# Optimization experiments

Hardware: AMD Instinct MI355X
Metric: run time of the kernel (lower is better)

## Reference

```python
import jax, jax.numpy as jnp
import numpy as np

B, H, NI, NO, T = 128, 256, 2, 10, 64
LAMBDA, ETA, SAMPLE, DECISION = 0.95, 0.5, 32, 8


def _xavier(key, shape):
    fan_in, fan_out = shape
    s = (2.0 / (fan_in + fan_out)) ** 0.5
    return jax.random.normal(key, shape, dtype=jnp.float32) * s


def setup_inputs():
    key = jax.random.key(0)
    ks = jax.random.split(key, 10)
    return {
        "x_in": jax.random.normal(ks[0], (T, B, 5), dtype=jnp.float32),
        "W_sr": _xavier(ks[1], (NI, H)),
        "W_ma": _xavier(ks[2], (NI + 1, H)),
        "W_ro": _xavier(ks[3], (H, H)),
        "W_ao": _xavier(ks[4], (H, H)),
        "W_ar": _xavier(ks[5], (H, H)),
        "W_ra": _xavier(ks[6], (H, H)),
        "W_a": _xavier(ks[7], (H, H)),
        "W_y": _xavier(ks[8], (H, NO)),
        "g": jnp.ones((1, H), dtype=jnp.float32),
        "b": jnp.zeros((1, H), dtype=jnp.float32),
        "time": T,
    }


def _forward(x_in, W_sr, W_ma, W_ro, W_ao, W_ar, W_ra, W_a, W_y, g, b):
    Tn = x_in.shape[0]

    def step(carry, inp):
        r, a, A = carry
        x, t = inp  # x: [B,5]
        a_prev = a
        # ATN / RSC recurrent populations
        a = jax.nn.relu(x[:, NI:] @ W_ma + a @ W_a + r @ W_ra)      # [B,H]
        r = jax.nn.relu(x[:, :NI] @ W_sr + a_prev @ W_ar)           # [B,H]
        # readout through fast-weight memory A: o = ro(r) + r @ A + ao(a)
        o = r @ W_ro + jnp.einsum('bh,bhk->bk', r, A) + a @ W_ao    # [B,H]
        mu = jnp.mean(o, axis=0, keepdims=True)                     # mean over batch
        o = jax.nn.relu(g * (o - mu) + b)
        # Hebbian fast-weight update: A = lambda*A + eta * outer(o, r)
        eta_t = jnp.where(t > SAMPLE, 0.0, ETA)
        A = LAMBDA * A + eta_t * o[:, :, None] * r[:, None, :]      # [B,H,H]
        y = o @ W_y                                                 # [B,NO]
        return (r, a, A), y

    carry0 = (
        jnp.zeros((B, H), jnp.float32),
        jnp.zeros((B, H), jnp.float32),
        jnp.zeros((B, H, H), jnp.float32),
    )
    _, ys = jax.lax.scan(step, carry0, (x_in, jnp.arange(Tn)))
    return ys[-DECISION:]  # [decision, B, n_output]


def reference(x_in, W_sr, W_ma, W_ro, W_ao, W_ar, W_ra, W_a, W_y, g, b, time):
    return _forward(x_in, W_sr, W_ma, W_ro, W_ao, W_ar, W_ra, W_a, W_y, g, b)
```

## Files before the change

kernel.cpp:

```cpp
#include <hip/hip_runtime.h>


typedef unsigned long long u64;

#define HH 256
#define NSTEPS 64

#define OFF_ST 0u
#define OFF_C  262144u
#define OFF_MU 329728u
#define WS_FLOATS 395264u

#define SENT_STATE   0xBF800000BF800000ull
#define SENT_C       0xBF800000u
#define SENT_MU      0x7FC00000u
#define SENT_MU_PAIR 0x7FC000007FC00000ull

#define AGENT __HIP_MEMORY_SCOPE_AGENT
#define RLX   __ATOMIC_RELAXED

__device__ __forceinline__ u64 ld64(const u64* p){ return __hip_atomic_load(p,RLX,AGENT); }
__device__ __forceinline__ void st64s(u64* p,u64 v){ __hip_atomic_store(p,v,RLX,AGENT); }
__device__ __forceinline__ float ld32f(const float* p){ return __hip_atomic_load(p,RLX,AGENT); }
__device__ __forceinline__ void st32f(float* p,float v){ __hip_atomic_store(p,v,RLX,AGENT); }
__device__ __forceinline__ u64 pack2(float lo,float hi){
  return (u64)__float_as_uint(lo) | ((u64)__float_as_uint(hi)<<32);
}

__global__ __launch_bounds__(256) void smn_init(float* __restrict__ ws,
                                                float* __restrict__ out){
  unsigned i = blockIdx.x*256u + threadIdx.x, st = gridDim.x*256u;
  u64* stp=(u64*)(ws+OFF_ST); float* cp=ws+OFF_C; u64* mp=(u64*)(ws+OFF_MU);
  for (unsigned k=i;k<131072u;k+=st) st64s(&stp[k],SENT_STATE);
  for (unsigned k=i;k<67584u;k+=st)  st32f(&cp[k],-1.0f);
  for (unsigned k=i;k<32768u;k+=st)  st64s(&mp[k],SENT_MU_PAIR);
  for (unsigned k=i;k<10240u;k+=st)  out[k]=0.f;
}

__global__ __launch_bounds__(512) void smn_main(
    const float* __restrict__ x_in, const float* __restrict__ W_sr,
    const float* __restrict__ W_ma, const float* __restrict__ W_ro,
    const float* __restrict__ W_ao, const float* __restrict__ W_ar,
    const float* __restrict__ W_ra, const float* __restrict__ W_a,
    const float* __restrict__ W_y,  const float* __restrict__ gvec,
    const float* __restrict__ bvec, float* __restrict__ out,
    float* __restrict__ ws)
{
  __shared__ __align__(16) float aF[2][HH], rF[2][HH];
  __shared__ __align__(16) float P[2][32][2][64];
  __shared__ __align__(16) float r_hist[33][2][64];
  __shared__ __align__(16) float o_hist[33][2][64];
  __shared__ float a_own[2][64], r_own[2][64];
  __shared__ float opre[2][64];
  __shared__ float c_l[33][2];
  __shared__ float mu_l[64];
  __shared__ float muG[16][32][2];
  __shared__ float lam_pow[64];
  __shared__ float x_l[2][5];
  __shared__ float lds_pad[8192];

  const int tid = threadIdx.x;
  const int bid = blockIdx.x;
  const int grp = bid >> 2, jsl = bid & 3;
  const int b0 = grp * 2, c0 = jsl * 64;
  const int q = tid & 15, ks = tid >> 4;

  u64*   st64    = (u64*)(ws + OFF_ST);
  float* c_parts = ws + OFF_C;
  u64*   mu64    = (u64*)(ws + OFF_MU);

  if (out == nullptr) lds_pad[tid] = 1.f;

  const int cc = c0 + (tid & 63);
  const float gv  = gvec[cc], bv = bvec[cc];
  const float wma0=W_ma[cc], wma1=W_ma[HH+cc], wma2=W_ma[2*HH+cc];
  const float wsr0=W_sr[cc], wsr1=W_sr[HH+cc];
  if (tid < 64) lam_pow[tid] = powf(0.95f,(float)tid);
  if (tid < 10) x_l[tid/5][tid%5] = x_in[(b0 + tid/5)*5 + tid%5];
  __syncthreads();

  for (int t = 0; t <= NSTEPS; ++t) {
    if (t < NSTEPS) {
      if (t == 0) {
        if (tid < 128) {
          int b = tid>>6, c = tid&63;
          float va = fmaxf(x_l[b][2]*wma0 + x_l[b][3]*wma1 + x_l[b][4]*wma2, 0.f);
          float vr = fmaxf(x_l[b][0]*wsr0 + x_l[b][1]*wsr1, 0.f);
          a_own[b][c]=va; r_own[b][c]=vr; r_hist[0][b][c]=vr;
          st64s(&st64[(unsigned)((b0+b)*HH + cc)], pack2(va,vr));
        }
        __syncthreads();
      } else {
        const int kb = ks*8;
        float sa0[8],sa1[8],sr0[8],sr1[8];
        *(float4*)&sa0[0]=*(const float4*)&aF[0][kb]; *(float4*)&sa0[4]=*(const float4*)&aF[0][kb+4];
        *(float4*)&sa1[0]=*(const float4*)&aF[1][kb]; *(float4*)&sa1[4]=*(const float4*)&aF[1][kb+4];
        *(float4*)&sr0[0]=*(const float4*)&rF[0][kb]; *(float4*)&sr0[4]=*(const float4*)&rF[0][kb+4];
        *(float4*)&sr1[0]=*(const float4*)&rF[1][kb]; *(float4*)&sr1[4]=*(const float4*)&rF[1][kb+4];
        float aA[2][4]={{0.f,0.f,0.f,0.f},{0.f,0.f,0.f,0.f}};
        float aR[2][4]={{0.f,0.f,0.f,0.f},{0.f,0.f,0.f,0.f}};
        #pragma unroll
        for (int kk=0; kk<8; ++kk) {
          const int k = kb + kk;
          const float4 wa = *(const float4*)&W_a [k*HH + c0 + q*4];
          const float4 wr = *(const float4*)&W_ra[k*HH + c0 + q*4];
          const float4 wn = *(const float4*)&W_ar[k*HH + c0 + q*4];
          #pragma unroll
          for (int jj=0;jj<4;++jj){
            const float waj=(&wa.x)[jj], wrj=(&wr.x)[jj], wnj=(&wn.x)[jj];
            aA[0][jj] += sa0[kk]*waj + sr0[kk]*wrj;
            aA[1][jj] += sa1[kk]*waj + sr1[kk]*wrj;
            aR[0][jj] += sa0[kk]*wnj;
            aR[1][jj] += sa1[kk]*wnj;
          }
        }
        *(float4*)&P[0][ks][0][q*4] = make_float4(aA[0][0],aA[0][1],aA[0][2],aA[0][3]);
        *(float4*)&P[0][ks][1][q*4] = make_float4(aA[1][0],aA[1][1],aA[1][2],aA[1][3]);
        *(float4*)&P[1][ks][0][q*4] = make_float4(aR[0][0],aR[0][1],aR[0][2],aR[0][3]);
        *(float4*)&P[1][ks][1][q*4] = make_float4(aR[1][0],aR[1][1],aR[1][2],aR[1][3]);
        __syncthreads();
        if (tid < 128) {
          int b=tid>>6, c=tid&63;
          float sa=0.f, sr=0.f;
          #pragma unroll
          for (int e=0;e<32;++e){ sa+=P[0][e][b][c]; sr+=P[1][e][b][c]; }
          float va = fmaxf(sa + x_l[b][2]*wma0 + x_l[b][3]*wma1 + x_l[b][4]*wma2, 0.f);
          float vr = fmaxf(sr + x_l[b][0]*wsr0 + x_l[b][1]*wsr1, 0.f);
          a_own[b][c]=va; r_own[b][c]=vr;
          if (t<=32) r_hist[t][b][c]=vr;
          st64s(&st64[(unsigned)((t&3)*32768) + (unsigned)((b0+b)*HH + cc)], pack2(va,vr));
        }
        __syncthreads();
      }
      if (t+1 < NSTEPS && tid < 10)
        x_l[tid/5][tid%5] = x_in[((t+1)*128 + b0 + tid/5)*5 + tid%5];
    }

    const int tp = t - 1;
    const bool fin = (t >= 1) && (tp <= 32 || tp >= 56);
    if (fin) {
      const int m = (tp <= 32) ? tp : tp - 23;
      {
        const int p = tid & 31, ch = tid >> 5;
        const u64* base = &mu64[(unsigned)(((m&3)*4 + jsl)*64) * 32u];
        float s0=0.f, s1=0.f;
        #pragma unroll
        for (int gg=0; gg<4; ++gg) {
          const u64* ptr = &base[(unsigned)((ch*4+gg)*32 + p)];
          u64 v;
          for (;;){ v = ld64(ptr);
            if ((unsigned)v != SENT_MU && (unsigned)(v>>32) != SENT_MU) break;
            __builtin_amdgcn_s_sleep(1);
          }
          s0 += __uint_as_float((unsigned)v);
          s1 += __uint_as_float((unsigned)(v>>32));
        }
        muG[ch][p][0]=s0; muG[ch][p][1]=s1;
      }
      __syncthreads();
      if (tid < 32) {
        float s0=0.f,s1=0.f;
        #pragma unroll
        for (int ch2=0;ch2<16;++ch2){ s0+=muG[ch2][tid][0]; s1+=muG[ch2][tid][1]; }
        mu_l[2*tid]=s0*(1.f/128.f); mu_l[2*tid+1]=s1*(1.f/128.f);
        st64s(&mu64[(unsigned)((((m+3)&3)*4 + jsl)*64 + grp)*32u + (unsigned)tid], SENT_MU_PAIR);
      }
      __syncthreads();
      if (tid < 128) {
        int b=tid>>6, c=tid&63;
        float o = fmaxf(gv*(opre[b][c]-mu_l[c]) + bv, 0.f);
        opre[b][c]=o;
        if (tp<=32) o_hist[tp][b][c]=o;
      }
      __syncthreads();
      if (tp >= 56 && tid < 320) {
        int ow=tid>>4, l16=tid&15, b=ow/10, n=ow%10;
        float acc=0.f;
        #pragma unroll
        for (int i2=0;i2<4;++i2){ int c=l16*4+i2; acc += opre[b][c]*W_y[(c0+c)*10+n]; }
        acc+=__shfl_xor(acc,1); acc+=__shfl_xor(acc,2);
        acc+=__shfl_xor(acc,4); acc+=__shfl_xor(acc,8);
        if (l16==0) atomicAdd(&out[(tp-56)*1280 + (b0+b)*10 + n], acc);
      }
    }
    if (t == NSTEPS) break;

    const bool live = (t <= 32 || t >= 56);
    const int mc = (t <= 32) ? t : t - 23;
    const int smax = (t-1 < 32) ? (t-1) : 32;

    if (tid < 128) {
      if (live && smax >= 0) {
        const int l8 = tid & 7;
        for (int pp = tid>>3; pp < (smax+1)*2; pp += 16) {
          const int s = pp>>1, b = pp&1;
          float acc=0.f;
          #pragma unroll
          for (int i2=0;i2<8;++i2){ int c=l8*8+i2; acc += r_own[b][c]*o_hist[s][b][c]; }
          acc+=__shfl_xor(acc,1); acc+=__shfl_xor(acc,2); acc+=__shfl_xor(acc,4);
          if (l8==0) st32f(&c_parts[(unsigned)((((mc&3)*33+s)*128 + b0+b)*4 + jsl)], acc);
        }
      }
      { int b=tid>>6, c=tid&63; aF[b][c0+c]=a_own[b][c]; rF[b][c0+c]=r_own[b][c]; }
    } else {
      const int w = tid - 128;
      const int pi = w >> 7, w2 = w & 127, b = w2>>6, c64 = w2&63;
      const int jp = (jsl + 1 + pi) & 3;
      const u64* ptr = &st64[(unsigned)((t&3)*32768) + (unsigned)((b0+b)*HH + jp*64 + c64)];
      u64 v;
      for (;;){ v = ld64(ptr); if (v != SENT_STATE) break; }
      aF[b][jp*64+c64] = __uint_as_float((unsigned)v);
      rF[b][jp*64+c64] = __uint_as_float((unsigned)(v>>32));
    }
    __syncthreads();
    if (tid < 128) {
      int b=tid>>6;
      st64s(&st64[(unsigned)(((t+3)&3)*32768) + (unsigned)((b0+b)*HH + cc)], SENT_STATE);
    }

    if (live) {
      const int kb = ks*8;
      float sa0[8],sa1[8],sr0[8],sr1[8];
      *(float4*)&sa0[0]=*(const float4*)&aF[0][kb]; *(float4*)&sa0[4]=*(const float4*)&aF[0][kb+4];
      *(float4*)&sa1[0]=*(const float4*)&aF[1][kb]; *(float4*)&sa1[4]=*(const float4*)&aF[1][kb+4];
      *(float4*)&sr0[0]=*(const float4*)&rF[0][kb]; *(float4*)&sr0[4]=*(const float4*)&rF[0][kb+4];
      *(float4*)&sr1[0]=*(const float4*)&rF[1][kb]; *(float4*)&sr1[4]=*(const float4*)&rF[1][kb+4];
      float aO[2][4]={{0.f,0.f,0.f,0.f},{0.f,0.f,0.f,0.f}};
      #pragma unroll
      for (int kk=0;kk<8;++kk){
        const int k=kb+kk;
        const float4 wo=*(const float4*)&W_ro[k*HH + c0 + q*4];
        const float4 wq=*(const float4*)&W_ao[k*HH + c0 + q*4];
        #pragma unroll
        for (int jj=0;jj<4;++jj){
          aO[0][jj] += sr0[kk]*(&wo.x)[jj] + sa0[kk]*(&wq.x)[jj];
          aO[1][jj] += sr1[kk]*(&wo.x)[jj] + sa1[kk]*(&wq.x)[jj];
        }
      }
      *(float4*)&P[0][ks][0][q*4] = make_float4(aO[0][0],aO[0][1],aO[0][2],aO[0][3]);
      *(float4*)&P[0][ks][1][q*4] = make_float4(aO[1][0],aO[1][1],aO[1][2],aO[1][3]);
      if (smax >= 0 && tid < (smax+1)*8) {
        const int s=tid>>3, b=(tid>>2)&1, jj2=tid&3;
        const float* ptr=&c_parts[(unsigned)((((mc&3)*33+s)*128 + b0+b)*4 + jj2)];
        float v;
        for(;;){ v=ld32f(ptr); if (__float_as_uint(v)!=SENT_C) break; }
        v+=__shfl_xor(v,1); v+=__shfl_xor(v,2);
        if (jj2==0) c_l[s][b]=v;
      }
      __syncthreads();
      if (smax >= 0 && tid >= 128 && tid < 194) {
        const int s=(tid-128)>>1, b=(tid-128)&1;
        st32f(&c_parts[(unsigned)(((((mc+3)&3)*33+s)*128 + b0+b)*4 + jsl)], -1.0f);
      }
      if (tid < 128) {
        int b=tid>>6, c=tid&63;
        float s=0.f;
        #pragma unroll
        for (int e=0;e<32;++e) s+=P[0][e][b][c];
        for (int s2=0;s2<=smax;++s2)
          s += lam_pow[t-1-s2]*0.5f*c_l[s2][b]*r_hist[s2][b][c];
        opre[b][c]=s;
      }
      __syncthreads();
      if (tid < 32) {
        float plo=opre[0][2*tid]+opre[1][2*tid];
        float phi=opre[0][2*tid+1]+opre[1][2*tid+1];
        st64s(&mu64[(unsigned)(((mc&3)*4 + jsl)*64 + grp)*32u + (unsigned)tid], pack2(plo,phi));
      }
    }
  }
}

extern "C" void kernel_launch(void* const* d_in, const int* in_sizes, int n_in,
                              void* d_out, int out_size, void* d_ws, size_t ws_size,
                              hipStream_t stream) {
  if (ws_size < (size_t)WS_FLOATS * 4) return;
  const float* x_in = (const float*)d_in[0];
  const float* W_sr = (const float*)d_in[1];
  const float* W_ma = (const float*)d_in[2];
  const float* W_ro = (const float*)d_in[3];
  const float* W_ao = (const float*)d_in[4];
  const float* W_ar = (const float*)d_in[5];
  const float* W_ra = (const float*)d_in[6];
  const float* W_a  = (const float*)d_in[7];
  const float* W_y  = (const float*)d_in[8];
  const float* g    = (const float*)d_in[9];
  const float* b    = (const float*)d_in[10];
  float* out = (float*)d_out;
  float* ws  = (float*)d_ws;

  hipLaunchKernelGGL(smn_init, dim3(256), dim3(256), 0, stream, ws, out);
  hipLaunchKernelGGL(smn_main, dim3(256), dim3(512), 0, stream,
                     x_in, W_sr, W_ma, W_ro, W_ao, W_ar, W_ra, W_a, W_y, g, b,
                     out, ws);
}
```

Measured before the change: 366.7 us.

## Split hidden dimension across 8 blocks per batch pair with smaller workgroups

Each batch pair's hidden columns are now split across 8 blocks of 256 threads, 32 columns each, instead of 4 blocks of 512 threads with 64 columns. The LDS padding array is removed so two workgroups can share a CU, and the launch grows to 512 blocks. Cross-block polling for state and mu now issues several independent loads per pass instead of one load with a sleep between retries. The intent is to cut per-block work on the serial recurrence critical path. The cost is more inter-block communication, since each block gathers 7 remote slices per step, and the reduction scratch buffers become twice as large.

```diff
diff --git a/kernel.cpp b/kernel.cpp
--- a/kernel.cpp
+++ b/kernel.cpp
@@ -8,8 +8,8 @@
 
 #define OFF_ST 0u
 #define OFF_C  262144u
-#define OFF_MU 329728u
-#define WS_FLOATS 395264u
+#define OFF_MU 397312u
+#define WS_FLOATS 462848u
 
 #define SENT_STATE   0xBF800000BF800000ull
 #define SENT_C       0xBF800000u
@@ -32,12 +32,12 @@
   unsigned i = blockIdx.x*256u + threadIdx.x, st = gridDim.x*256u;
   u64* stp=(u64*)(ws+OFF_ST); float* cp=ws+OFF_C; u64* mp=(u64*)(ws+OFF_MU);
   for (unsigned k=i;k<131072u;k+=st) st64s(&stp[k],SENT_STATE);
-  for (unsigned k=i;k<67584u;k+=st)  st32f(&cp[k],-1.0f);
+  for (unsigned k=i;k<135168u;k+=st) st32f(&cp[k],__uint_as_float(SENT_C));
   for (unsigned k=i;k<32768u;k+=st)  st64s(&mp[k],SENT_MU_PAIR);
   for (unsigned k=i;k<10240u;k+=st)  out[k]=0.f;
 }
 
-__global__ __launch_bounds__(512) void smn_main(
+__global__ __launch_bounds__(256,2) void smn_main(
     const float* __restrict__ x_in, const float* __restrict__ W_sr,
     const float* __restrict__ W_ma, const float* __restrict__ W_ro,
     const float* __restrict__ W_ao, const float* __restrict__ W_ar,
@@ -47,34 +47,30 @@
     float* __restrict__ ws)
 {
   __shared__ __align__(16) float aF[2][HH], rF[2][HH];
-  __shared__ __align__(16) float P[2][32][2][64];
-  __shared__ __align__(16) float r_hist[33][2][64];
-  __shared__ __align__(16) float o_hist[33][2][64];
-  __shared__ float a_own[2][64], r_own[2][64];
-  __shared__ float opre[2][64];
+  __shared__ __align__(16) float P[2][32][2][32];
+  __shared__ __align__(16) float r_hist[33][2][32];
+  __shared__ __align__(16) float o_hist[33][2][32];
+  __shared__ float opre[2][32];
   __shared__ float c_l[33][2];
-  __shared__ float mu_l[64];
-  __shared__ float muG[16][32][2];
+  __shared__ float mu_l[32];
+  __shared__ float muG[16][16][2];
   __shared__ float lam_pow[64];
   __shared__ float x_l[2][5];
-  __shared__ float lds_pad[8192];
 
   const int tid = threadIdx.x;
   const int bid = blockIdx.x;
-  const int grp = bid >> 2, jsl = bid & 3;
-  const int b0 = grp * 2, c0 = jsl * 64;
-  const int q = tid & 15, ks = tid >> 4;
+  const int grp = bid >> 3, jsl = bid & 7;
+  const int b0 = grp * 2, c0 = jsl * 32;
+  const int q = tid & 7, ks = tid >> 3;
 
   u64*   st64    = (u64*)(ws + OFF_ST);
   float* c_parts = ws + OFF_C;
   u64*   mu64    = (u64*)(ws + OFF_MU);
 
-  if (out == nullptr) lds_pad[tid] = 1.f;
-
-  const int cc = c0 + (tid & 63);
-  const float gv  = gvec[cc], bv = bvec[cc];
-  const float wma0=W_ma[cc], wma1=W_ma[HH+cc], wma2=W_ma[2*HH+cc];
-  const float wsr0=W_sr[cc], wsr1=W_sr[HH+cc];
+  const int cc2 = c0 + (tid & 31);
+  const float gv  = gvec[cc2], bv = bvec[cc2];
+  const float wma0=W_ma[cc2], wma1=W_ma[HH+cc2], wma2=W_ma[2*HH+cc2];
+  const float wsr0=W_sr[cc2], wsr1=W_sr[HH+cc2];
   if (tid < 64) lam_pow[tid] = powf(0.95f,(float)tid);
   if (tid < 10) x_l[tid/5][tid%5] = x_in[(b0 + tid/5)*5 + tid%5];
   __syncthreads();
@@ -82,12 +78,12 @@
   for (int t = 0; t <= NSTEPS; ++t) {
     if (t < NSTEPS) {
       if (t == 0) {
-        if (tid < 128) {
-          int b = tid>>6, c = tid&63;
+        if (tid < 64) {
+          int b = tid>>5, c = tid&31;
           float va = fmaxf(x_l[b][2]*wma0 + x_l[b][3]*wma1 + x_l[b][4]*wma2, 0.f);
           float vr = fmaxf(x_l[b][0]*wsr0 + x_l[b][1]*wsr1, 0.f);
-          a_own[b][c]=va; r_own[b][c]=vr; r_hist[0][b][c]=vr;
-          st64s(&st64[(unsigned)((b0+b)*HH + cc)], pack2(va,vr));
+          aF[b][c0+c]=va; rF[b][c0+c]=vr; r_hist[0][b][c]=vr;
+          st64s(&st64[(unsigned)((b0+b)*HH + cc2)], pack2(va,vr));
         }
         __syncthreads();
       } else {
@@ -119,16 +115,16 @@
         *(float4*)&P[1][ks][0][q*4] = make_float4(aR[0][0],aR[0][1],aR[0][2],aR[0][3]);
         *(float4*)&P[1][ks][1][q*4] = make_float4(aR[1][0],aR[1][1],aR[1][2],aR[1][3]);
         __syncthreads();
-        if (tid < 128) {
-          int b=tid>>6, c=tid&63;
+        if (tid < 64) {
+          int b=tid>>5, c=tid&31;
           float sa=0.f, sr=0.f;
           #pragma unroll
           for (int e=0;e<32;++e){ sa+=P[0][e][b][c]; sr+=P[1][e][b][c]; }
           float va = fmaxf(sa + x_l[b][2]*wma0 + x_l[b][3]*wma1 + x_l[b][4]*wma2, 0.f);
           float vr = fmaxf(sr + x_l[b][0]*wsr0 + x_l[b][1]*wsr1, 0.f);
-          a_own[b][c]=va; r_own[b][c]=vr;
           if (t<=32) r_hist[t][b][c]=vr;
-          st64s(&st64[(unsigned)((t&3)*32768) + (unsigned)((b0+b)*HH + cc)], pack2(va,vr));
+          st64s(&st64[(unsigned)((t&3)*32768) + (unsigned)((b0+b)*HH + cc2)], pack2(va,vr));
+          aF[b][c0+c]=va; rF[b][c0+c]=vr;
         }
         __syncthreads();
       }
@@ -141,46 +137,51 @@
     if (fin) {
       const int m = (tp <= 32) ? tp : tp - 23;
       {
-        const int p = tid & 31, ch = tid >> 5;
-        const u64* base = &mu64[(unsigned)(((m&3)*4 + jsl)*64) * 32u];
+        const int p = tid & 15, ch = tid >> 4;
+        const u64* base = &mu64[(unsigned)(((m&3)*8 + jsl)*64)*16u];
+        u64 vals[4]; unsigned rm = 0;
+        const u64* ptrs[4];
+        #pragma unroll
+        for (int gg=0; gg<4; ++gg) ptrs[gg] = &base[(unsigned)((ch*4+gg)*16 + p)];
+        while (rm != 0xFu) {
+          #pragma unroll
+          for (int gg=0; gg<4; ++gg) if (!(rm & (1u<<gg))) {
+            u64 v = ld64(ptrs[gg]);
+            if ((unsigned)v != SENT_MU && (unsigned)(v>>32) != SENT_MU) { vals[gg]=v; rm |= 1u<<gg; }
+          }
+        }
         float s0=0.f, s1=0.f;
         #pragma unroll
-        for (int gg=0; gg<4; ++gg) {
-          const u64* ptr = &base[(unsigned)((ch*4+gg)*32 + p)];
-          u64 v;
-          for (;;){ v = ld64(ptr);
-            if ((unsigned)v != SENT_MU && (unsigned)(v>>32) != SENT_MU) break;
-            __builtin_amdgcn_s_sleep(1);
-          }
-          s0 += __uint_as_float((unsigned)v);
-          s1 += __uint_as_float((unsigned)(v>>32));
-        }
+        for (int gg=0; gg<4; ++gg) { s0 += __uint_as_float((unsigned)vals[gg]);
+                                     s1 += __uint_as_float((unsigned)(vals[gg]>>32)); }
         muG[ch][p][0]=s0; muG[ch][p][1]=s1;
       }
       __syncthreads();
-      if (tid < 32) {
+      if (tid < 16) {
         float s0=0.f,s1=0.f;
         #pragma unroll
         for (int ch2=0;ch2<16;++ch2){ s0+=muG[ch2][tid][0]; s1+=muG[ch2][tid][1]; }
         mu_l[2*tid]=s0*(1.f/128.f); mu_l[2*tid+1]=s1*(1.f/128.f);
-        st64s(&mu64[(unsigned)((((m+3)&3)*4 + jsl)*64 + grp)*32u + (unsigned)tid], SENT_MU_PAIR);
-      }
-      __syncthreads();
-      if (tid < 128) {
-        int b=tid>>6, c=tid&63;
+        st64s(&mu64[(unsigned)((((m+3)&3)*8 + jsl)*64 + grp)*16u + (unsigned)tid], SENT_MU_PAIR);
+      }
+      __syncthreads();
+      if (tid < 64) {
+        int b=tid>>5, c=tid&31;
         float o = fmaxf(gv*(opre[b][c]-mu_l[c]) + bv, 0.f);
         opre[b][c]=o;
         if (tp<=32) o_hist[tp][b][c]=o;
       }
       __syncthreads();
-      if (tp >= 56 && tid < 320) {
-        int ow=tid>>4, l16=tid&15, b=ow/10, n=ow%10;
-        float acc=0.f;
-        #pragma unroll
-        for (int i2=0;i2<4;++i2){ int c=l16*4+i2; acc += opre[b][c]*W_y[(c0+c)*10+n]; }
-        acc+=__shfl_xor(acc,1); acc+=__shfl_xor(acc,2);
-        acc+=__shfl_xor(acc,4); acc+=__shfl_xor(acc,8);
-        if (l16==0) atomicAdd(&out[(tp-56)*1280 + (b0+b)*10 + n], acc);
+      if (tp >= 56) {
+        const int pr = tid>>3, l8 = tid&7;
+        if (pr < 20) {
+          const int b = pr/10, n = pr%10;
+          float acc=0.f;
+          #pragma unroll
+          for (int i2=0;i2<4;++i2){ int c=l8*4+i2; acc += opre[b][c]*W_y[(c0+c)*10+n]; }
+          acc+=__shfl_xor(acc,1); acc+=__shfl_xor(acc,2); acc+=__shfl_xor(acc,4);
+          if (l8==0) atomicAdd(&out[(tp-56)*1280 + (b0+b)*10 + n], acc);
+        }
       }
     }
     if (t == NSTEPS) break;
@@ -189,33 +190,52 @@
     const int mc = (t <= 32) ? t : t - 23;
     const int smax = (t-1 < 32) ? (t-1) : 32;
 
-    if (tid < 128) {
-      if (live && smax >= 0) {
-        const int l8 = tid & 7;
-        for (int pp = tid>>3; pp < (smax+1)*2; pp += 16) {
+    const int gbase = live ? 128 : 0;
+    if (live && tid < 128) {
+      if (smax >= 0) {
+        const int l4 = tid & 3;
+        for (int pp = tid>>2; pp < (smax+1)*2; pp += 32) {
           const int s = pp>>1, b = pp&1;
           float acc=0.f;
           #pragma unroll
-          for (int i2=0;i2<8;++i2){ int c=l8*8+i2; acc += r_own[b][c]*o_hist[s][b][c]; }
-          acc+=__shfl_xor(acc,1); acc+=__shfl_xor(acc,2); acc+=__shfl_xor(acc,4);
-          if (l8==0) st32f(&c_parts[(unsigned)((((mc&3)*33+s)*128 + b0+b)*4 + jsl)], acc);
-        }
-      }
-      { int b=tid>>6, c=tid&63; aF[b][c0+c]=a_own[b][c]; rF[b][c0+c]=r_own[b][c]; }
-    } else {
-      const int w = tid - 128;
-      const int pi = w >> 7, w2 = w & 127, b = w2>>6, c64 = w2&63;
-      const int jp = (jsl + 1 + pi) & 3;
-      const u64* ptr = &st64[(unsigned)((t&3)*32768) + (unsigned)((b0+b)*HH + jp*64 + c64)];
-      u64 v;
-      for (;;){ v = ld64(ptr); if (v != SENT_STATE) break; }
-      aF[b][jp*64+c64] = __uint_as_float((unsigned)v);
-      rF[b][jp*64+c64] = __uint_as_float((unsigned)(v>>32));
+          for (int i2=0;i2<8;++i2){ int c=l4*8+i2; acc += rF[b][c0+c]*o_hist[s][b][c]; }
+          acc+=__shfl_xor(acc,1); acc+=__shfl_xor(acc,2);
+          if (l4==0) st32f(&c_parts[(unsigned)((((mc&3)*33+s)*128 + b0+b)*8 + jsl)], acc);
+        }
+      }
+    }
+    if (tid >= gbase) {
+      const int gstep = live ? 128 : 256;
+      const int w0 = tid - gbase;
+      const u64* ptrs[4]; int bs[4], cs[4]; bool ok[4];
+      u64 vals[4]; unsigned rm = 0;
+      #pragma unroll
+      for (int i=0;i<4;++i) {
+        int w = w0 + i*gstep;
+        bool valid = (w < 512);
+        int b = (w>>8)&1, c = w&255;
+        ok[i] = valid && ((c>>5) != jsl);
+        bs[i]=b; cs[i]=c;
+        ptrs[i] = &st64[(unsigned)((t&3)*32768) + (unsigned)((b0+b)*HH + c)];
+        if (!ok[i]) rm |= 1u<<i;
+      }
+      while (rm != 0xFu) {
+        #pragma unroll
+        for (int i=0;i<4;++i) if (!(rm & (1u<<i))) {
+          u64 v = ld64(ptrs[i]);
+          if (v != SENT_STATE) { vals[i]=v; rm |= 1u<<i; }
+        }
+      }
+      #pragma unroll
+      for (int i=0;i<4;++i) if (ok[i]) {
+        aF[bs[i]][cs[i]] = __uint_as_float((unsigned)vals[i]);
+        rF[bs[i]][cs[i]] = __uint_as_float((unsigned)(vals[i]>>32));
+      }
     }
     __syncthreads();
-    if (tid < 128) {
-      int b=tid>>6;
-      st64s(&st64[(unsigned)(((t+3)&3)*32768) + (unsigned)((b0+b)*HH + cc)], SENT_STATE);
+    if (tid < 64) {
+      int b=tid>>5;
+      st64s(&st64[(unsigned)(((t+3)&3)*32768) + (unsigned)((b0+b)*HH + cc2)], SENT_STATE);
     }
 
     if (live) {
@@ -239,21 +259,25 @@
       }
       *(float4*)&P[0][ks][0][q*4] = make_float4(aO[0][0],aO[0][1],aO[0][2],aO[0][3]);
       *(float4*)&P[0][ks][1][q*4] = make_float4(aO[1][0],aO[1][1],aO[1][2],aO[1][3]);
-      if (smax >= 0 && tid < (smax+1)*8) {
-        const int s=tid>>3, b=(tid>>2)&1, jj2=tid&3;
-        const float* ptr=&c_parts[(unsigned)((((mc&3)*33+s)*128 + b0+b)*4 + jj2)];
-        float v;
-        for(;;){ v=ld32f(ptr); if (__float_as_uint(v)!=SENT_C) break; }
-        v+=__shfl_xor(v,1); v+=__shfl_xor(v,2);
-        if (jj2==0) c_l[s][b]=v;
-      }
-      __syncthreads();
-      if (smax >= 0 && tid >= 128 && tid < 194) {
-        const int s=(tid-128)>>1, b=(tid-128)&1;
-        st32f(&c_parts[(unsigned)(((((mc+3)&3)*33+s)*128 + b0+b)*4 + jsl)], -1.0f);
-      }
-      if (tid < 128) {
-        int b=tid>>6, c=tid&63;
+      if (smax >= 0) {
+        const int jj2 = tid & 7;
+        for (int pp = tid>>3; pp < (smax+1)*2; pp += 32) {
+          const int s=pp>>1, b=pp&1;
+          const float* ptr=&c_parts[(unsigned)((((mc&3)*33+s)*128 + b0+b)*8 + jj2)];
+          float v;
+          for(;;){ v=ld32f(ptr); if (__float_as_uint(v)!=SENT_C) break; }
+          v+=__shfl_xor(v,1); v+=__shfl_xor(v,2); v+=__shfl_xor(v,4);
+          if (jj2==0) c_l[s][b]=v;
+        }
+      }
+      __syncthreads();
+      if (smax >= 0 && tid >= 64 && tid < 64 + (smax+1)*2) {
+        const int s=(tid-64)>>1, b=(tid-64)&1;
+        st32f(&c_parts[(unsigned)(((((mc+3)&3)*33+s)*128 + b0+b)*8 + jsl)],
+              __uint_as_float(SENT_C));
+      }
+      if (tid < 64) {
+        int b=tid>>5, c=tid&31;
         float s=0.f;
         #pragma unroll
         for (int e=0;e<32;++e) s+=P[0][e][b][c];
@@ -262,10 +286,10 @@
         opre[b][c]=s;
       }
       __syncthreads();
-      if (tid < 32) {
+      if (tid < 16) {
         float plo=opre[0][2*tid]+opre[1][2*tid];
         float phi=opre[0][2*tid+1]+opre[1][2*tid+1];
-        st64s(&mu64[(unsigned)(((mc&3)*4 + jsl)*64 + grp)*32u + (unsigned)tid], pack2(plo,phi));
+        st64s(&mu64[(unsigned)(((mc&3)*8 + jsl)*64 + grp)*16u + (unsigned)tid], pack2(plo,phi));
       }
     }
   }
@@ -290,7 +314,7 @@
   float* ws  = (float*)d_ws;
 
   hipLaunchKernelGGL(smn_init, dim3(256), dim3(256), 0, stream, ws, out);
-  hipLaunchKernelGGL(smn_main, dim3(256), dim3(512), 0, stream,
+  hipLaunchKernelGGL(smn_main, dim3(512), dim3(256), 0, stream,
                      x_in, W_sr, W_ma, W_ro, W_ao, W_ar, W_ra, W_a, W_y, g, b,
                      out, ws);
 }
```

New measurement: 482.1 us. +31.5%, slower.

## Reschedule cross-block exchange, prefetch readout weights, and use lighter LDS barriers

Applied to the files above, without the earlier changes.

Reorders the per-step schedule so the state exchange and the Hebbian c-partial computation run before the mean reduction rather than after. The readout weights W_ro/W_ao are prefetched into registers ahead of the mu spin-wait, and sentinel resets are moved to the producer side two slots ahead. The four mu slots are polled concurrently without sleeping. Several __syncthreads calls become an s_waitcnt lgkmcnt(0) plus s_barrier, and launch bounds now request two blocks per SIMD. The goal is shorter critical-path latency per timestep in this spin-synchronised persistent kernel. The cost is more register pressure and fragile ordering of the sentinel protocol.

```diff
diff --git a/kernel.cpp b/kernel.cpp
--- a/kernel.cpp
+++ b/kernel.cpp
@@ -18,6 +18,8 @@
 
 #define AGENT __HIP_MEMORY_SCOPE_AGENT
 #define RLX   __ATOMIC_RELAXED
+
+#define BAR_LGKM() asm volatile("s_waitcnt lgkmcnt(0)\ns_barrier" ::: "memory")
 
 __device__ __forceinline__ u64 ld64(const u64* p){ return __hip_atomic_load(p,RLX,AGENT); }
 __device__ __forceinline__ void st64s(u64* p,u64 v){ __hip_atomic_store(p,v,RLX,AGENT); }
@@ -32,12 +34,12 @@
   unsigned i = blockIdx.x*256u + threadIdx.x, st = gridDim.x*256u;
   u64* stp=(u64*)(ws+OFF_ST); float* cp=ws+OFF_C; u64* mp=(u64*)(ws+OFF_MU);
   for (unsigned k=i;k<131072u;k+=st) st64s(&stp[k],SENT_STATE);
-  for (unsigned k=i;k<67584u;k+=st)  st32f(&cp[k],-1.0f);
+  for (unsigned k=i;k<67584u;k+=st)  st32f(&cp[k],__uint_as_float(SENT_C));
   for (unsigned k=i;k<32768u;k+=st)  st64s(&mp[k],SENT_MU_PAIR);
   for (unsigned k=i;k<10240u;k+=st)  out[k]=0.f;
 }
 
-__global__ __launch_bounds__(512) void smn_main(
+__global__ __launch_bounds__(512,2) void smn_main(
     const float* __restrict__ x_in, const float* __restrict__ W_sr,
     const float* __restrict__ W_ma, const float* __restrict__ W_ro,
     const float* __restrict__ W_ao, const float* __restrict__ W_ar,
@@ -50,7 +52,6 @@
   __shared__ __align__(16) float P[2][32][2][64];
   __shared__ __align__(16) float r_hist[33][2][64];
   __shared__ __align__(16) float o_hist[33][2][64];
-  __shared__ float a_own[2][64], r_own[2][64];
   __shared__ float opre[2][64];
   __shared__ float c_l[33][2];
   __shared__ float mu_l[64];
@@ -71,25 +72,29 @@
 
   if (out == nullptr) lds_pad[tid] = 1.f;
 
-  const int cc = c0 + (tid & 63);
-  const float gv  = gvec[cc], bv = bvec[cc];
-  const float wma0=W_ma[cc], wma1=W_ma[HH+cc], wma2=W_ma[2*HH+cc];
-  const float wsr0=W_sr[cc], wsr1=W_sr[HH+cc];
+  const int cc2 = c0 + (tid & 63);
+  const float gv  = gvec[cc2], bv = bvec[cc2];
+  const float wma0=W_ma[cc2], wma1=W_ma[HH+cc2], wma2=W_ma[2*HH+cc2];
+  const float wsr0=W_sr[cc2], wsr1=W_sr[HH+cc2];
   if (tid < 64) lam_pow[tid] = powf(0.95f,(float)tid);
   if (tid < 10) x_l[tid/5][tid%5] = x_in[(b0 + tid/5)*5 + tid%5];
   __syncthreads();
 
   for (int t = 0; t <= NSTEPS; ++t) {
+    const bool live = (t <= 32 || t >= 56);
+    const int mc = (t <= 32) ? t : t - 23;
+
     if (t < NSTEPS) {
       if (t == 0) {
         if (tid < 128) {
           int b = tid>>6, c = tid&63;
           float va = fmaxf(x_l[b][2]*wma0 + x_l[b][3]*wma1 + x_l[b][4]*wma2, 0.f);
           float vr = fmaxf(x_l[b][0]*wsr0 + x_l[b][1]*wsr1, 0.f);
-          a_own[b][c]=va; r_own[b][c]=vr; r_hist[0][b][c]=vr;
-          st64s(&st64[(unsigned)((b0+b)*HH + cc)], pack2(va,vr));
-        }
-        __syncthreads();
+          aF[b][c0+c]=va; rF[b][c0+c]=vr; r_hist[0][b][c]=vr;
+          st64s(&st64[(unsigned)(2*32768) + (unsigned)((b0+b)*HH + cc2)], SENT_STATE);
+          st64s(&st64[(unsigned)((b0+b)*HH + cc2)], pack2(va,vr));
+        }
+        BAR_LGKM();
       } else {
         const int kb = ks*8;
         float sa0[8],sa1[8],sr0[8],sr1[8];
@@ -118,7 +123,7 @@
         *(float4*)&P[0][ks][1][q*4] = make_float4(aA[1][0],aA[1][1],aA[1][2],aA[1][3]);
         *(float4*)&P[1][ks][0][q*4] = make_float4(aR[0][0],aR[0][1],aR[0][2],aR[0][3]);
         *(float4*)&P[1][ks][1][q*4] = make_float4(aR[1][0],aR[1][1],aR[1][2],aR[1][3]);
-        __syncthreads();
+        BAR_LGKM();
         if (tid < 128) {
           int b=tid>>6, c=tid&63;
           float sa=0.f, sr=0.f;
@@ -126,38 +131,82 @@
           for (int e=0;e<32;++e){ sa+=P[0][e][b][c]; sr+=P[1][e][b][c]; }
           float va = fmaxf(sa + x_l[b][2]*wma0 + x_l[b][3]*wma1 + x_l[b][4]*wma2, 0.f);
           float vr = fmaxf(sr + x_l[b][0]*wsr0 + x_l[b][1]*wsr1, 0.f);
-          a_own[b][c]=va; r_own[b][c]=vr;
           if (t<=32) r_hist[t][b][c]=vr;
-          st64s(&st64[(unsigned)((t&3)*32768) + (unsigned)((b0+b)*HH + cc)], pack2(va,vr));
-        }
-        __syncthreads();
+          st64s(&st64[(unsigned)(((t+2)&3)*32768) + (unsigned)((b0+b)*HH + cc2)], SENT_STATE);
+          st64s(&st64[(unsigned)((t&3)*32768) + (unsigned)((b0+b)*HH + cc2)], pack2(va,vr));
+          aF[b][c0+c]=va; rF[b][c0+c]=vr;
+        }
+        BAR_LGKM();
       }
       if (t+1 < NSTEPS && tid < 10)
         x_l[tid/5][tid%5] = x_in[((t+1)*128 + b0 + tid/5)*5 + tid%5];
     }
 
+    float4 woR[8], wqR[8];
+    if (t < NSTEPS && live) {
+      const int kb = ks*8;
+      #pragma unroll
+      for (int kk=0;kk<8;++kk){
+        woR[kk] = *(const float4*)&W_ro[(kb+kk)*HH + c0 + q*4];
+        wqR[kk] = *(const float4*)&W_ao[(kb+kk)*HH + c0 + q*4];
+      }
+    }
+
+    if (t < NSTEPS) {
+      const int smax_old = ((t-2) < 32) ? (t-2) : 32;
+      if (tid < 128) {
+        if (live && smax_old >= 0) {
+          const int l8 = tid & 7;
+          for (int pp = tid>>3; pp < (smax_old+1)*2; pp += 16) {
+            const int s = pp>>1, b2 = pp&1;
+            float acc=0.f;
+            #pragma unroll
+            for (int i2=0;i2<8;++i2){ int c=l8*8+i2; acc += rF[b2][c0+c]*o_hist[s][b2][c]; }
+            acc+=__shfl_xor(acc,1); acc+=__shfl_xor(acc,2); acc+=__shfl_xor(acc,4);
+            if (l8==0) {
+              st32f(&c_parts[(unsigned)(((((mc+2)&3)*33+s)*128 + b0+b2)*4 + jsl)],
+                    __uint_as_float(SENT_C));
+              st32f(&c_parts[(unsigned)((((mc&3)*33+s)*128 + b0+b2)*4 + jsl)], acc);
+            }
+          }
+        }
+      } else {
+        const int w = tid - 128;
+        const int pi = w >> 7, w2 = w & 127, b = w2>>6, c64 = w2&63;
+        const int jp = (jsl + 1 + pi) & 3;
+        const u64* ptr = &st64[(unsigned)((t&3)*32768) + (unsigned)((b0+b)*HH + jp*64 + c64)];
+        u64 v;
+        for (;;){ v = ld64(ptr); if (v != SENT_STATE) break; }
+        aF[b][jp*64+c64] = __uint_as_float((unsigned)v);
+        rF[b][jp*64+c64] = __uint_as_float((unsigned)(v>>32));
+      }
+      if (live) { BAR_LGKM(); } else { __syncthreads(); }
+    }
+
     const int tp = t - 1;
-    const bool fin = (t >= 1) && (tp <= 32 || tp >= 56);
-    if (fin) {
+    if (t >= 1 && (tp <= 32 || tp >= 56)) {
       const int m = (tp <= 32) ? tp : tp - 23;
       {
         const int p = tid & 31, ch = tid >> 5;
-        const u64* base = &mu64[(unsigned)(((m&3)*4 + jsl)*64) * 32u];
+        const u64* base = &mu64[(unsigned)(((m&3)*4 + jsl)*64)*32u];
+        u64 vals[4]; unsigned rm = 0;
+        const u64* ptrs[4];
+        #pragma unroll
+        for (int gg=0; gg<4; ++gg) ptrs[gg] = &base[(unsigned)((ch*4+gg)*32 + p)];
+        while (rm != 0xFu) {
+          #pragma unroll
+          for (int gg=0; gg<4; ++gg) if (!(rm & (1u<<gg))) {
+            u64 v = ld64(ptrs[gg]);
+            if ((unsigned)v != SENT_MU && (unsigned)(v>>32) != SENT_MU) { vals[gg]=v; rm |= 1u<<gg; }
+          }
+        }
         float s0=0.f, s1=0.f;
         #pragma unroll
-        for (int gg=0; gg<4; ++gg) {
-          const u64* ptr = &base[(unsigned)((ch*4+gg)*32 + p)];
-          u64 v;
-          for (;;){ v = ld64(ptr);
-            if ((unsigned)v != SENT_MU && (unsigned)(v>>32) != SENT_MU) break;
-            __builtin_amdgcn_s_sleep(1);
-          }
-          s0 += __uint_as_float((unsigned)v);
-          s1 += __uint_as_float((unsigned)(v>>32));
-        }
+        for (int gg=0; gg<4; ++gg) { s0 += __uint_as_float((unsigned)vals[gg]);
+                                     s1 += __uint_as_float((unsigned)(vals[gg]>>32)); }
         muG[ch][p][0]=s0; muG[ch][p][1]=s1;
       }
-      __syncthreads();
+      BAR_LGKM();
       if (tid < 32) {
         float s0=0.f,s1=0.f;
         #pragma unroll
@@ -165,14 +214,14 @@
         mu_l[2*tid]=s0*(1.f/128.f); mu_l[2*tid+1]=s1*(1.f/128.f);
         st64s(&mu64[(unsigned)((((m+3)&3)*4 + jsl)*64 + grp)*32u + (unsigned)tid], SENT_MU_PAIR);
       }
-      __syncthreads();
+      BAR_LGKM();
       if (tid < 128) {
         int b=tid>>6, c=tid&63;
         float o = fmaxf(gv*(opre[b][c]-mu_l[c]) + bv, 0.f);
         opre[b][c]=o;
         if (tp<=32) o_hist[tp][b][c]=o;
       }
-      __syncthreads();
+      BAR_LGKM();
       if (tp >= 56 && tid < 320) {
         int ow=tid>>4, l16=tid&15, b=ow/10, n=ow%10;
         float acc=0.f;
@@ -185,37 +234,19 @@
     }
     if (t == NSTEPS) break;
 
-    const bool live = (t <= 32 || t >= 56);
-    const int mc = (t <= 32) ? t : t - 23;
-    const int smax = (t-1 < 32) ? (t-1) : 32;
-
-    if (tid < 128) {
-      if (live && smax >= 0) {
-        const int l8 = tid & 7;
-        for (int pp = tid>>3; pp < (smax+1)*2; pp += 16) {
-          const int s = pp>>1, b = pp&1;
-          float acc=0.f;
-          #pragma unroll
-          for (int i2=0;i2<8;++i2){ int c=l8*8+i2; acc += r_own[b][c]*o_hist[s][b][c]; }
-          acc+=__shfl_xor(acc,1); acc+=__shfl_xor(acc,2); acc+=__shfl_xor(acc,4);
-          if (l8==0) st32f(&c_parts[(unsigned)((((mc&3)*33+s)*128 + b0+b)*4 + jsl)], acc);
-        }
-      }
-      { int b=tid>>6, c=tid&63; aF[b][c0+c]=a_own[b][c]; rF[b][c0+c]=r_own[b][c]; }
-    } else {
-      const int w = tid - 128;
-      const int pi = w >> 7, w2 = w & 127, b = w2>>6, c64 = w2&63;
-      const int jp = (jsl + 1 + pi) & 3;
-      const u64* ptr = &st64[(unsigned)((t&3)*32768) + (unsigned)((b0+b)*HH + jp*64 + c64)];
-      u64 v;
-      for (;;){ v = ld64(ptr); if (v != SENT_STATE) break; }
-      aF[b][jp*64+c64] = __uint_as_float((unsigned)v);
-      rF[b][jp*64+c64] = __uint_as_float((unsigned)(v>>32));
-    }
-    __syncthreads();
-    if (tid < 128) {
-      int b=tid>>6;
-      st64s(&st64[(unsigned)(((t+3)&3)*32768) + (unsigned)((b0+b)*HH + cc)], SENT_STATE);
+    if (live && t >= 1 && t <= 33) {
+      if (tid < 16) {
+        const int s = t-1, b2 = tid>>3, l8 = tid&7;
+        float acc=0.f;
+        #pragma unroll
+        for (int i2=0;i2<8;++i2){ int c=l8*8+i2; acc += rF[b2][c0+c]*o_hist[s][b2][c]; }
+        acc+=__shfl_xor(acc,1); acc+=__shfl_xor(acc,2); acc+=__shfl_xor(acc,4);
+        if (l8==0) {
+          st32f(&c_parts[(unsigned)(((((mc+2)&3)*33+s)*128 + b0+b2)*4 + jsl)],
+                __uint_as_float(SENT_C));
+          st32f(&c_parts[(unsigned)((((mc&3)*33+s)*128 + b0+b2)*4 + jsl)], acc);
+        }
+      }
     }
 
     if (live) {
@@ -228,30 +259,25 @@
       float aO[2][4]={{0.f,0.f,0.f,0.f},{0.f,0.f,0.f,0.f}};
       #pragma unroll
       for (int kk=0;kk<8;++kk){
-        const int k=kb+kk;
-        const float4 wo=*(const float4*)&W_ro[k*HH + c0 + q*4];
-        const float4 wq=*(const float4*)&W_ao[k*HH + c0 + q*4];
         #pragma unroll
         for (int jj=0;jj<4;++jj){
-          aO[0][jj] += sr0[kk]*(&wo.x)[jj] + sa0[kk]*(&wq.x)[jj];
-          aO[1][jj] += sr1[kk]*(&wo.x)[jj] + sa1[kk]*(&wq.x)[jj];
+          const float woj=(&woR[kk].x)[jj], wqj=(&wqR[kk].x)[jj];
+          aO[0][jj] += sr0[kk]*woj + sa0[kk]*wqj;
+          aO[1][jj] += sr1[kk]*woj + sa1[kk]*wqj;
         }
       }
       *(float4*)&P[0][ks][0][q*4] = make_float4(aO[0][0],aO[0][1],aO[0][2],aO[0][3]);
       *(float4*)&P[0][ks][1][q*4] = make_float4(aO[1][0],aO[1][1],aO[1][2],aO[1][3]);
+      const int smax = (t-1 < 32) ? (t-1) : 32;
       if (smax >= 0 && tid < (smax+1)*8) {
-        const int s=tid>>3, b=(tid>>2)&1, jj2=tid&3;
-        const float* ptr=&c_parts[(unsigned)((((mc&3)*33+s)*128 + b0+b)*4 + jj2)];
+        const int s=tid>>3, b2=(tid>>2)&1, jj2=tid&3;
+        const float* ptr=&c_parts[(unsigned)((((mc&3)*33+s)*128 + b0+b2)*4 + jj2)];
         float v;
         for(;;){ v=ld32f(ptr); if (__float_as_uint(v)!=SENT_C) break; }
         v+=__shfl_xor(v,1); v+=__shfl_xor(v,2);
-        if (jj2==0) c_l[s][b]=v;
+        if (jj2==0) c_l[s][b2]=v;
       }
       __syncthreads();
-      if (smax >= 0 && tid >= 128 && tid < 194) {
-        const int s=(tid-128)>>1, b=(tid-128)&1;
-        st32f(&c_parts[(unsigned)(((((mc+3)&3)*33+s)*128 + b0+b)*4 + jsl)], -1.0f);
-      }
       if (tid < 128) {
         int b=tid>>6, c=tid&63;
         float s=0.f;
@@ -261,7 +287,7 @@
           s += lam_pow[t-1-s2]*0.5f*c_l[s2][b]*r_hist[s2][b][c];
         opre[b][c]=s;
       }
-      __syncthreads();
+      BAR_LGKM();
       if (tid < 32) {
         float plo=opre[0][2*tid]+opre[1][2*tid];
         float phi=opre[0][2*tid+1]+opre[1][2*tid+1];
```

Measured after the change: 492.1 us. 34.2% more time.
